# Kernel optimization log

Hardware: AMD Instinct MI355X
Metric: run time of the kernel (lower is better)

## Reference

```python
import jax, jax.numpy as jnp
import numpy as np

N = 50000
E_RAND = 800000
F_IN = 512
HID = 64
HEADS = 4
C = 40
NEG_SLOPE = 0.2  # PyG GATConv default leaky_relu slope


def setup_inputs() -> dict:
    key = jax.random.key(0)
    ks = jax.random.split(key, 12)
    x = jax.random.normal(ks[0], (N, F_IN), dtype=jnp.float32)
    # random edges + self loops (PyG GATConv add_self_loops=True)
    ei_rand = jax.random.randint(ks[1], (2, E_RAND), 0, N, dtype=jnp.int64)
    loops = jnp.broadcast_to(jnp.arange(N, dtype=jnp.int64), (2, N))
    edge_index = jnp.concatenate([ei_rand, loops], axis=1)  # [2, 850000]
    # layer 1: F_IN -> HEADS*HID, concat
    s1 = 1.0 / np.sqrt(F_IN)
    W1 = jax.random.normal(ks[2], (F_IN, HEADS * HID), dtype=jnp.float32) * s1
    a_src1 = jax.random.normal(ks[3], (HEADS, HID), dtype=jnp.float32) * (1.0 / np.sqrt(HID))
    a_dst1 = jax.random.normal(ks[4], (HEADS, HID), dtype=jnp.float32) * (1.0 / np.sqrt(HID))
    b1 = jnp.zeros((HEADS * HID,), dtype=jnp.float32)
    # layer 2: HEADS*HID -> C, 1 head, concat=False
    s2 = 1.0 / np.sqrt(HEADS * HID)
    W2 = jax.random.normal(ks[5], (HEADS * HID, C), dtype=jnp.float32) * s2
    a_src2 = jax.random.normal(ks[6], (1, C), dtype=jnp.float32) * (1.0 / np.sqrt(C))
    a_dst2 = jax.random.normal(ks[7], (1, C), dtype=jnp.float32) * (1.0 / np.sqrt(C))
    b2 = jnp.zeros((C,), dtype=jnp.float32)
    return {"x": x, "edge_index": edge_index, "W1": W1, "a_src1": a_src1,
            "a_dst1": a_dst1, "b1": b1, "W2": W2, "a_src2": a_src2,
            "a_dst2": a_dst2, "b2": b2}


def gat_conv(x, src, dst, W, a_s, a_d, b, concat):
    n = x.shape[0]
    H, D = a_s.shape
    h = (x @ W).reshape(n, H, D)                    # [N,H,D]
    al_s = jnp.einsum('nhd,hd->nh', h, a_s)          # per-node src score
    al_d = jnp.einsum('nhd,hd->nh', h, a_d)          # per-node dst score
    e = jax.nn.leaky_relu(al_s[src] + al_d[dst], NEG_SLOPE)  # [E,H]
    # segment softmax over edges grouped by destination node
    m = jax.ops.segment_max(e, dst, num_segments=n)  # [N,H]
    e = jnp.exp(e - m[dst])
    denom = jax.ops.segment_sum(e, dst, num_segments=n)
    alpha = e / (denom[dst] + 1e-16)                 # [E,H]
    msg = h[src] * alpha[:, :, None]                 # [E,H,D]
    out = jax.ops.segment_sum(msg, dst, num_segments=n)  # [N,H,D]
    out = out.reshape(n, H * D) if concat else out.mean(axis=1)
    return out + b


def reference(x, edge_index, W1, a_src1, a_dst1, b1, W2, a_src2, a_dst2, b2):
    src, dst = edge_index[0], edge_index[1]
    # dropout p=0.6 is identity in eval mode
    h = jax.nn.elu(gat_conv(x, src, dst, W1, a_src1, a_dst1, b1, concat=True))
    out = gat_conv(h, src, dst, W2, a_src2, a_dst2, b2, concat=False)
    return jax.nn.log_softmax(out, axis=1)
```

## Files before the change

kernel.cpp:

```cpp
#include <hip/hip_runtime.h>
#include <math.h>

#define NNODES 50000
#define FIN 512
#define HID 64
#define HEADS 4
#define HD (HEADS * HID)
#define NCLS 40
#define NCLSP 64
#define NEG_SLOPE 0.2f
#define SBLK 256
#define NSCAN ((NNODES + SBLK - 1) / SBLK)

#define W1TBLK (FIN * HD / 256)
#define W2TBLK NCLSP

typedef __attribute__((ext_vector_type(8))) short short8;
typedef __attribute__((ext_vector_type(4))) float f32x4;

static __device__ inline unsigned short f2bf(float f) {
    unsigned int u = __builtin_bit_cast(unsigned int, f);
    unsigned int r = (u + 0x7FFFu + ((u >> 16) & 1u)) >> 16;
    return (unsigned short)r;
}
static __device__ inline float bf2f(unsigned short b) {
    return __builtin_bit_cast(float, (unsigned int)b << 16);
}
static __device__ inline void gload_lds16(const unsigned short* g, unsigned short* l) {
    __builtin_amdgcn_global_load_lds(
        (const __attribute__((address_space(1))) unsigned int*)g,
        (__attribute__((address_space(3))) unsigned int*)l, 16, 0, 0);
}

__global__ __launch_bounds__(256) void pre_kernel(const float* __restrict__ W1,
                                                  unsigned short* __restrict__ W1t,
                                                  const float* __restrict__ W2,
                                                  unsigned short* __restrict__ W2t,
                                                  const int* __restrict__ ei, int E, int eb,
                                                  int* __restrict__ deg,
                                                  int* __restrict__ csr_pad) {
    const int b = blockIdx.x;
    const int tid = threadIdx.x;
    if (b < eb) {
        const int e = b * 256 + tid;
        if (e < E) atomicAdd(&deg[ei[E + e]], 1);
        if (b == 0 && tid < 64) csr_pad[tid] = 0;
    } else if (b < eb + W1TBLK) {
        const int idx = (b - eb) * 256 + tid;
        const int k = idx >> 8;
        const int n = idx & 255;
        W1t[n * FIN + k] = f2bf(W1[idx]);
    } else {
        const int idx = (b - eb - W1TBLK) * 256 + tid;
        const int n = idx >> 8;
        const int k = idx & 255;
        W2t[n * HD + k] = (n < NCLS) ? f2bf(W2[k * NCLS + n]) : (unsigned short)0;
    }
}

#define BM 64
#define BN 256
#define BK 32
#define G1BLK ((NNODES + BM - 1) / BM)

__global__ __launch_bounds__(256) void gemm1_kernel(const float* __restrict__ x,
                                                    const unsigned short* __restrict__ W1t,
                                                    const float* __restrict__ a_src,
                                                    const float* __restrict__ a_dst,
                                                    unsigned short* __restrict__ h1,
                                                    float* __restrict__ al_s,
                                                    float* __restrict__ al_d) {
    __shared__ unsigned short As[2][BM * BK];
    __shared__ unsigned short Bs[2][BN * BK];
    const int tid = threadIdx.x;
    const int wave = tid >> 6;
    const int lane = tid & 63;
    const int quad = lane >> 4;
    const int col = lane & 15;
    const int m0 = blockIdx.x * BM;
    const int srow = lane >> 2;
    const int skk = (lane & 3) * 8;

    const int ar = wave * 16 + srow;
    const size_t agr = (size_t)min(m0 + ar, NNODES - 1) * FIN;

    f32x4 acc[4][4] = {};

    auto stageB = [&](int buf, int k0) {
        #pragma unroll
        for (int c = 0; c < 4; ++c) {
            const int rr = c * 64 + wave * 16 + srow;
            gload_lds16(&W1t[(size_t)rr * FIN + k0 + skk], &Bs[buf][rr * BK + skk]);
        }
    };
    auto stageA = [&](int buf, int k0) {
        const float4 v0 = *(const float4*)&x[agr + k0 + skk];
        const float4 v1 = *(const float4*)&x[agr + k0 + skk + 4];
        short8 p;
        p[0] = (short)f2bf(v0.x); p[1] = (short)f2bf(v0.y);
        p[2] = (short)f2bf(v0.z); p[3] = (short)f2bf(v0.w);
        p[4] = (short)f2bf(v1.x); p[5] = (short)f2bf(v1.y);
        p[6] = (short)f2bf(v1.z); p[7] = (short)f2bf(v1.w);
        *(short8*)&As[buf][ar * BK + skk] = p;
    };
    auto compute = [&](int buf) {
        short8 af[4], bfv[4];
        #pragma unroll
        for (int i = 0; i < 4; ++i)
            af[i] = *(const short8*)&As[buf][(i * 16 + col) * BK + quad * 8];
        #pragma unroll
        for (int j = 0; j < 4; ++j)
            bfv[j] = *(const short8*)&Bs[buf][(wave * 64 + j * 16 + col) * BK + quad * 8];
        #pragma unroll
        for (int i = 0; i < 4; ++i)
            #pragma unroll
            for (int j = 0; j < 4; ++j)
                acc[i][j] = __builtin_amdgcn_mfma_f32_16x16x32_bf16(af[i], bfv[j], acc[i][j], 0, 0, 0);
    };

    stageB(0, 0);
    stageA(0, 0);
    __syncthreads();
    int cur = 0;
    for (int k0 = BK; k0 < FIN; k0 += BK) {
        stageB(cur ^ 1, k0);
        stageA(cur ^ 1, k0);
        compute(cur);
        __syncthreads();
        cur ^= 1;
    }
    compute(cur);

    float asv[4], adv[4];
    #pragma unroll
    for (int j = 0; j < 4; ++j) {
        asv[j] = a_src[wave * 64 + j * 16 + col];
        adv[j] = a_dst[wave * 64 + j * 16 + col];
    }
    #pragma unroll
    for (int i = 0; i < 4; ++i) {
        #pragma unroll
        for (int reg = 0; reg < 4; ++reg) {
            const int row = i * 16 + quad * 4 + reg;
            const int gm = m0 + row;
            float ds = 0.f, dd = 0.f;
            #pragma unroll
            for (int j = 0; j < 4; ++j) {
                const float v = acc[i][j][reg];
                ds = fmaf(v, asv[j], ds);
                dd = fmaf(v, adv[j], dd);
                if (gm < NNODES) {
                    const int gc = wave * 64 + j * 16 + col;
                    h1[(size_t)gm * HD + gc] = f2bf(v);
                }
            }
            #pragma unroll
            for (int off = 1; off < 16; off <<= 1) {
                ds += __shfl_xor(ds, off);
                dd += __shfl_xor(dd, off);
            }
            if (col == 0 && gm < NNODES) {
                al_s[gm * HEADS + wave] = ds;
                al_d[gm * HEADS + wave] = dd;
            }
        }
    }
}

__global__ __launch_bounds__(SBLK) void scan1_kernel(const int* __restrict__ deg,
                                                     int* __restrict__ psum,
                                                     int* __restrict__ bsum) {
    __shared__ int ws[4];
    const int t = threadIdx.x;
    const int idx = blockIdx.x * SBLK + t;
    const int lane = t & 63;
    const int w = t >> 6;
    int sv = (idx < NNODES) ? deg[idx] : 0;
    #pragma unroll
    for (int off = 1; off < 64; off <<= 1) {
        const int n = __shfl_up(sv, off);
        if (lane >= off) sv += n;
    }
    if (lane == 63) ws[w] = sv;
    __syncthreads();
    int add = 0;
    for (int i = 0; i < w; ++i) add += ws[i];
    sv += add;
    if (idx < NNODES) psum[idx] = sv;
    if (t == SBLK - 1) bsum[blockIdx.x] = sv;
}

__global__ __launch_bounds__(SBLK) void scan23_kernel(const int* __restrict__ deg,
                                                      const int* __restrict__ psum,
                                                      const int* __restrict__ bsum,
                                                      int* __restrict__ offsets) {
    __shared__ int ws[4];
    __shared__ int sc[NSCAN];
    const int t = threadIdx.x;
    const int lane = t & 63;
    const int w = t >> 6;
    int sv = (t < NSCAN) ? bsum[t] : 0;
    #pragma unroll
    for (int off = 1; off < 64; off <<= 1) {
        const int n = __shfl_up(sv, off);
        if (lane >= off) sv += n;
    }
    if (lane == 63) ws[w] = sv;
    __syncthreads();
    int add = 0;
    for (int i = 0; i < w; ++i) add += ws[i];
    sv += add;
    if (t < NSCAN) sc[t] = sv;
    __syncthreads();
    const int idx = blockIdx.x * SBLK + t;
    const int boff = (blockIdx.x > 0) ? sc[blockIdx.x - 1] : 0;
    if (idx < NNODES) offsets[idx] = psum[idx] - deg[idx] + boff;
    if (blockIdx.x == 0 && t == 0) offsets[NNODES] = sc[NSCAN - 1];
}

__global__ void scatter_kernel(const int* __restrict__ ei, int E,
                               const int* __restrict__ offsets,
                               int* __restrict__ cursor,
                               int* __restrict__ csr_src) {
    const int e = blockIdx.x * 256 + threadIdx.x;
    if (e < E) {
        const int dst = ei[E + e];
        const int src = ei[e];
        const int pos = offsets[dst] + atomicAdd(&cursor[dst], 1);
        csr_src[pos] = src;
    }
}

__global__ __launch_bounds__(256) void agg1_kernel(const unsigned short* __restrict__ h1,
                                                   const float* __restrict__ al_s,
                                                   const float* __restrict__ al_d,
                                                   const int* __restrict__ offsets,
                                                   const int* __restrict__ csr_src,
                                                   const float* __restrict__ b1,
                                                   unsigned short* __restrict__ h_act) {
    const int node = (blockIdx.x * 256 + threadIdx.x) >> 6;
    const int lane = threadIdx.x & 63;
    const int q = lane >> 4;
    const int fl = lane & 15;
    const int h = fl >> 2;
    const float ad = al_d[node * HEADS + h];
    const int start = offsets[node];
    const int end = offsets[node + 1];

    float s = 0.f;
    float acc[16] = {};

    {
        const int idx = start + q;
        const int src0 = csr_src[idx];
        float sc = (idx < end) ? al_s[src0 * HEADS + h] : -__builtin_inff();
        short8 v0 = *(const short8*)&h1[(size_t)src0 * HD + fl * 16];
        short8 v1 = *(const short8*)&h1[(size_t)src0 * HD + fl * 16 + 8];

        for (int i = start; i < end; i += 4) {
            const int j = i + 4 + q;
            const int nsrc = csr_src[j];
            const float nsc = (j < end) ? al_s[nsrc * HEADS + h] : -__builtin_inff();
            const short8 nv0 = *(const short8*)&h1[(size_t)nsrc * HD + fl * 16];
            const short8 nv1 = *(const short8*)&h1[(size_t)nsrc * HD + fl * 16 + 8];
            float e_ = sc + ad;
            e_ = e_ > 0.f ? e_ : NEG_SLOPE * e_;
            const float p = __expf(e_);
            s += p;
            #pragma unroll
            for (int k = 0; k < 8; ++k)
                acc[k] = fmaf(p, bf2f((unsigned short)v0[k]), acc[k]);
            #pragma unroll
            for (int k = 0; k < 8; ++k)
                acc[8 + k] = fmaf(p, bf2f((unsigned short)v1[k]), acc[8 + k]);
            sc = nsc; v0 = nv0; v1 = nv1;
        }
    }
    s += __shfl_xor(s, 16);
    s += __shfl_xor(s, 32);
    #pragma unroll
    for (int k = 0; k < 16; ++k) {
        acc[k] += __shfl_xor(acc[k], 16);
        acc[k] += __shfl_xor(acc[k], 32);
    }

    if (q == 0) {
        const float inv = 1.f / (s + 1e-16f);
        float bb[16];
        *(float4*)&bb[0]  = *(const float4*)&b1[fl * 16];
        *(float4*)&bb[4]  = *(const float4*)&b1[fl * 16 + 4];
        *(float4*)&bb[8]  = *(const float4*)&b1[fl * 16 + 8];
        *(float4*)&bb[12] = *(const float4*)&b1[fl * 16 + 12];
        short8 ob0, ob1;
        #pragma unroll
        for (int k = 0; k < 8; ++k) {
            const float o0 = acc[k] * inv + bb[k];
            const float o1 = acc[8 + k] * inv + bb[8 + k];
            const float e0 = o0 > 0.f ? o0 : expm1f(o0);
            const float e1 = o1 > 0.f ? o1 : expm1f(o1);
            ob0[k] = (short)f2bf(e0);
            ob1[k] = (short)f2bf(e1);
        }
        *(short8*)&h_act[(size_t)node * HD + fl * 16] = ob0;
        *(short8*)&h_act[(size_t)node * HD + fl * 16 + 8] = ob1;
    }
}

#define G2M 64
#define BSTRIDE 264

__global__ __launch_bounds__(256) void gemm2_kernel(const unsigned short* __restrict__ h_act,
                                                    const unsigned short* __restrict__ W2t,
                                                    const float* __restrict__ a_s2,
                                                    const float* __restrict__ a_d2,
                                                    unsigned short* __restrict__ h2,
                                                    float* __restrict__ al_s,
                                                    float* __restrict__ al_d) {
    __shared__ unsigned short Bt[NCLSP][BSTRIDE];
    const int tid = threadIdx.x;
    const int wave = tid >> 6;
    const int lane = tid & 63;
    const int quad = lane >> 4;
    const int col = lane & 15;
    const int m0 = blockIdx.x * G2M;

    #pragma unroll
    for (int it = 0; it < 8; ++it) {
        const int ch = it * 256 + tid;
        const int n = ch >> 5;
        const int c8 = (ch & 31) * 8;
        *(uint4*)&Bt[n][c8] = *(const uint4*)&W2t[(size_t)n * HD + c8];
    }

    const int rowm = m0 + wave * 16 + col;
    const int arow = min(rowm, NNODES - 1);
    short8 af[8];
    #pragma unroll
    for (int ks = 0; ks < 8; ++ks)
        af[ks] = *(const short8*)&h_act[(size_t)arow * HD + ks * 32 + quad * 8];

    __syncthreads();

    f32x4 acc[4] = {};
    #pragma unroll
    for (int j = 0; j < 4; ++j) {
        #pragma unroll
        for (int ks = 0; ks < 8; ++ks) {
            const short8 bfr = *(const short8*)&Bt[j * 16 + col][ks * 32 + quad * 8];
            acc[j] = __builtin_amdgcn_mfma_f32_16x16x32_bf16(af[ks], bfr, acc[j], 0, 0, 0);
        }
    }

    float ps[4] = {0.f, 0.f, 0.f, 0.f};
    float pd[4] = {0.f, 0.f, 0.f, 0.f};
    #pragma unroll
    for (int j = 0; j < 4; ++j) {
        const int c = j * 16 + col;
        const bool cv = c < NCLS;
        const float asc = cv ? a_s2[c] : 0.f;
        const float adc = cv ? a_d2[c] : 0.f;
        #pragma unroll
        for (int reg = 0; reg < 4; ++reg) {
            const float v = acc[j][reg];
            ps[reg] += v * asc;
            pd[reg] += v * adc;
            const int node = m0 + wave * 16 + quad * 4 + reg;
            if (node < NNODES)
                h2[(size_t)node * NCLSP + c] = f2bf(v);
        }
    }
    #pragma unroll
    for (int reg = 0; reg < 4; ++reg) {
        #pragma unroll
        for (int off = 1; off < 16; off <<= 1) {
            ps[reg] += __shfl_xor(ps[reg], off);
            pd[reg] += __shfl_xor(pd[reg], off);
        }
    }
    if (col == 0) {
        #pragma unroll
        for (int reg = 0; reg < 4; ++reg) {
            const int node = m0 + wave * 16 + quad * 4 + reg;
            if (node < NNODES) {
                al_s[node] = ps[reg];
                al_d[node] = pd[reg];
            }
        }
    }
}

__global__ __launch_bounds__(256) void agg2_kernel(const unsigned short* __restrict__ h2,
                                                   const float* __restrict__ al_s,
                                                   const float* __restrict__ al_d,
                                                   const int* __restrict__ offsets,
                                                   const int* __restrict__ csr_src,
                                                   const float* __restrict__ b2,
                                                   float* __restrict__ out) {
    const int node = (blockIdx.x * 256 + threadIdx.x) >> 6;
    const int lane = threadIdx.x & 63;
    const int oct = lane >> 3;
    const int fl = lane & 7;
    const float ad = al_d[node];
    const int start = offsets[node];
    const int end = offsets[node + 1];

    float s = 0.f;
    float acc[8] = {};

    {
        const int idx = start + oct;
        const int src0 = csr_src[idx];
        float sc = (idx < end) ? al_s[src0] : -__builtin_inff();
        short8 v = *(const short8*)&h2[(size_t)src0 * NCLSP + fl * 8];

        for (int i = start; i < end; i += 8) {
            const int j = i + 8 + oct;
            const int nsrc = csr_src[j];
            const float nsc = (j < end) ? al_s[nsrc] : -__builtin_inff();
            const short8 nv = *(const short8*)&h2[(size_t)nsrc * NCLSP + fl * 8];
            float e_ = sc + ad;
            e_ = e_ > 0.f ? e_ : NEG_SLOPE * e_;
            const float p = __expf(e_);
            s += p;
            #pragma unroll
            for (int k = 0; k < 8; ++k)
                acc[k] = fmaf(p, bf2f((unsigned short)v[k]), acc[k]);
            sc = nsc; v = nv;
        }
    }
    s += __shfl_xor(s, 8);
    s += __shfl_xor(s, 16);
    s += __shfl_xor(s, 32);
    #pragma unroll
    for (int k = 0; k < 8; ++k) {
        acc[k] += __shfl_xor(acc[k], 8);
        acc[k] += __shfl_xor(acc[k], 16);
        acc[k] += __shfl_xor(acc[k], 32);
    }

    if (oct == 0) {
        const float inv = 1.f / (s + 1e-16f);
        float o[8];
        float mx = -1e30f;
        #pragma unroll
        for (int k = 0; k < 8; ++k) {
            const int c = fl * 8 + k;
            const float bc = (c < NCLS) ? b2[c] : 0.f;
            o[k] = acc[k] * inv + bc;
            if (c < NCLS) mx = fmaxf(mx, o[k]);
        }
        #pragma unroll
        for (int off = 1; off < 8; off <<= 1) mx = fmaxf(mx, __shfl_xor(mx, off));
        float ex = 0.f;
        #pragma unroll
        for (int k = 0; k < 8; ++k) {
            const int c = fl * 8 + k;
            if (c < NCLS) ex += __expf(o[k] - mx);
        }
        #pragma unroll
        for (int off = 1; off < 8; off <<= 1) ex += __shfl_xor(ex, off);
        const float lse = mx + logf(ex);
        if (fl < 5) {
            float4 r0, r1;
            r0.x = o[0] - lse; r0.y = o[1] - lse; r0.z = o[2] - lse; r0.w = o[3] - lse;
            r1.x = o[4] - lse; r1.y = o[5] - lse; r1.z = o[6] - lse; r1.w = o[7] - lse;
            *(float4*)&out[(size_t)node * NCLS + fl * 8] = r0;
            *(float4*)&out[(size_t)node * NCLS + fl * 8 + 4] = r1;
        }
    }
}

extern "C" void kernel_launch(void* const* d_in, const int* in_sizes, int n_in,
                              void* d_out, int out_size, void* d_ws, size_t ws_size,
                              hipStream_t stream) {
    const float* x      = (const float*)d_in[0];
    const int*   ei     = (const int*)d_in[1];
    const float* W1     = (const float*)d_in[2];
    const float* a_src1 = (const float*)d_in[3];
    const float* a_dst1 = (const float*)d_in[4];
    const float* b1     = (const float*)d_in[5];
    const float* W2     = (const float*)d_in[6];
    const float* a_src2 = (const float*)d_in[7];
    const float* a_dst2 = (const float*)d_in[8];
    const float* b2     = (const float*)d_in[9];
    float* out = (float*)d_out;
    const int E = in_sizes[1] / 2;

    char* ws = (char*)d_ws;
    size_t off = 0;
    auto alloc = [&](size_t bytes) -> char* {
        char* p = ws + off;
        off += (bytes + 255) & ~(size_t)255;
        return p;
    };
    unsigned short* W1t   = (unsigned short*)alloc((size_t)FIN * HD * 2);
    unsigned short* W2t   = (unsigned short*)alloc((size_t)NCLSP * HD * 2);
    unsigned short* h1    = (unsigned short*)alloc((size_t)NNODES * HD * 2);
    unsigned short* h_act = (unsigned short*)alloc((size_t)NNODES * HD * 2);
    unsigned short* h2    = (unsigned short*)alloc((size_t)NNODES * NCLSP * 2);
    float* al_s1  = (float*)alloc((size_t)NNODES * HEADS * 4);
    float* al_d1  = (float*)alloc((size_t)NNODES * HEADS * 4);
    float* al_s2  = (float*)alloc((size_t)NNODES * 4);
    float* al_d2  = (float*)alloc((size_t)NNODES * 4);
    int*   deg    = (int*)alloc((size_t)NNODES * 4);
    int*   cursor = (int*)alloc((size_t)NNODES * 4);
    int*   psum   = (int*)alloc((size_t)NNODES * 4);
    int*   bsum   = (int*)alloc((size_t)SBLK * 4);
    int*   offs   = (int*)alloc((size_t)(NNODES + 1) * 4);
    int*   csrsrc = (int*)alloc((size_t)E * 4 + 256);

    const size_t degpad = ((size_t)NNODES * 4 + 255) & ~(size_t)255;
    hipMemsetAsync(deg, 0, degpad + (size_t)NNODES * 4, stream);

    const int eb = (E + 255) / 256;
    pre_kernel<<<eb + W1TBLK + W2TBLK, 256, 0, stream>>>(W1, W1t, W2, W2t, ei, E, eb, deg, csrsrc + E);
    scan1_kernel<<<NSCAN, SBLK, 0, stream>>>(deg, psum, bsum);
    scan23_kernel<<<NSCAN, SBLK, 0, stream>>>(deg, psum, bsum, offs);
    scatter_kernel<<<eb, 256, 0, stream>>>(ei, E, offs, cursor, csrsrc);

    gemm1_kernel<<<G1BLK, 256, 0, stream>>>(x, W1t, a_src1, a_dst1, h1, al_s1, al_d1);
    agg1_kernel<<<NNODES / 4, 256, 0, stream>>>(h1, al_s1, al_d1, offs, csrsrc, b1, h_act);
    gemm2_kernel<<<(NNODES + G2M - 1) / G2M, 256, 0, stream>>>(h_act, W2t, a_src2, a_dst2, h2, al_s2, al_d2);
    agg2_kernel<<<NNODES / 4, 256, 0, stream>>>(h2, al_s2, al_d2, offs, csrsrc, b2, out);
}
```

Baseline: 405.8 us.

## Stage fp32 x tile via direct global-to-LDS loads with XOR swizzle; cheaper bf16 unpack

The first GEMM now loads the fp32 input tile straight into LDS with asynchronous global_load_lds and an XOR-swizzled layout, and converts to bf16 when fragments are read rather than in registers before the LDS store. This takes the A-operand global loads off the VGPR path and lets them overlap with compute like the B tile does, at the price of twice the LDS footprint for A and conversion work repeated inside the compute loop. Separately, the layer-1 aggregation kernel unpacks bf16 pairs from 32-bit words with shift and mask instead of extracting individual shorts, which cuts unpack instructions.

New measurement: 401.1 us. About the same (-1.2%).

```diff
diff --git a/kernel.cpp b/kernel.cpp
--- a/kernel.cpp
+++ b/kernel.cpp
@@ -26,7 +26,7 @@
 static __device__ inline float bf2f(unsigned short b) {
     return __builtin_bit_cast(float, (unsigned int)b << 16);
 }
-static __device__ inline void gload_lds16(const unsigned short* g, unsigned short* l) {
+static __device__ inline void gload_lds16(const void* g, void* l) {
     __builtin_amdgcn_global_load_lds(
         (const __attribute__((address_space(1))) unsigned int*)g,
         (__attribute__((address_space(3))) unsigned int*)l, 16, 0, 0);
@@ -70,7 +70,7 @@
                                                     unsigned short* __restrict__ h1,
                                                     float* __restrict__ al_s,
                                                     float* __restrict__ al_d) {
-    __shared__ unsigned short As[2][BM * BK];
+    __shared__ float As32[2][BM * BK];
     __shared__ unsigned short Bs[2][BN * BK];
     const int tid = threadIdx.x;
     const int wave = tid >> 6;
@@ -80,12 +80,20 @@
     const int m0 = blockIdx.x * BM;
     const int srow = lane >> 2;
     const int skk = (lane & 3) * 8;
-
-    const int ar = wave * 16 + srow;
-    const size_t agr = (size_t)min(m0 + ar, NNODES - 1) * FIN;
+    const int l3 = lane >> 3;
+    const int ch = lane & 7;
+    const int chs = ch ^ l3;
 
     f32x4 acc[4][4] = {};
 
+    auto stageA = [&](int buf, int k0) {
+        #pragma unroll
+        for (int j = 0; j < 2; ++j) {
+            const int row = wave * 16 + j * 8 + l3;
+            const size_t rg = (size_t)min(m0 + row, NNODES - 1) * FIN;
+            gload_lds16(&x[rg + k0 + chs * 4], &As32[buf][row * BK + ch * 4]);
+        }
+    };
     auto stageB = [&](int buf, int k0) {
         #pragma unroll
         for (int c = 0; c < 4; ++c) {
@@ -93,21 +101,21 @@
             gload_lds16(&W1t[(size_t)rr * FIN + k0 + skk], &Bs[buf][rr * BK + skk]);
         }
     };
-    auto stageA = [&](int buf, int k0) {
-        const float4 v0 = *(const float4*)&x[agr + k0 + skk];
-        const float4 v1 = *(const float4*)&x[agr + k0 + skk + 4];
-        short8 p;
-        p[0] = (short)f2bf(v0.x); p[1] = (short)f2bf(v0.y);
-        p[2] = (short)f2bf(v0.z); p[3] = (short)f2bf(v0.w);
-        p[4] = (short)f2bf(v1.x); p[5] = (short)f2bf(v1.y);
-        p[6] = (short)f2bf(v1.z); p[7] = (short)f2bf(v1.w);
-        *(short8*)&As[buf][ar * BK + skk] = p;
-    };
     auto compute = [&](int buf) {
+        const int r7 = col & 7;
         short8 af[4], bfv[4];
         #pragma unroll
-        for (int i = 0; i < 4; ++i)
-            af[i] = *(const short8*)&As[buf][(i * 16 + col) * BK + quad * 8];
+        for (int i = 0; i < 4; ++i) {
+            const int row = i * 16 + col;
+            const float4 f0 = *(const float4*)&As32[buf][row * BK + (((2 * quad)     ^ r7) << 2)];
+            const float4 f1 = *(const float4*)&As32[buf][row * BK + (((2 * quad + 1) ^ r7) << 2)];
+            short8 p;
+            p[0] = (short)f2bf(f0.x); p[1] = (short)f2bf(f0.y);
+            p[2] = (short)f2bf(f0.z); p[3] = (short)f2bf(f0.w);
+            p[4] = (short)f2bf(f1.x); p[5] = (short)f2bf(f1.y);
+            p[6] = (short)f2bf(f1.z); p[7] = (short)f2bf(f1.w);
+            af[i] = p;
+        }
         #pragma unroll
         for (int j = 0; j < 4; ++j)
             bfv[j] = *(const short8*)&Bs[buf][(wave * 64 + j * 16 + col) * BK + quad * 8];
@@ -118,13 +126,13 @@
                 acc[i][j] = __builtin_amdgcn_mfma_f32_16x16x32_bf16(af[i], bfv[j], acc[i][j], 0, 0, 0);
     };
 
+    stageA(0, 0);
     stageB(0, 0);
-    stageA(0, 0);
     __syncthreads();
     int cur = 0;
     for (int k0 = BK; k0 < FIN; k0 += BK) {
+        stageA(cur ^ 1, k0);
         stageB(cur ^ 1, k0);
-        stageA(cur ^ 1, k0);
         compute(cur);
         __syncthreads();
         cur ^= 1;
@@ -254,25 +262,27 @@
         const int idx = start + q;
         const int src0 = csr_src[idx];
         float sc = (idx < end) ? al_s[src0 * HEADS + h] : -__builtin_inff();
-        short8 v0 = *(const short8*)&h1[(size_t)src0 * HD + fl * 16];
-        short8 v1 = *(const short8*)&h1[(size_t)src0 * HD + fl * 16 + 8];
+        uint4 v0 = *(const uint4*)&h1[(size_t)src0 * HD + fl * 16];
+        uint4 v1 = *(const uint4*)&h1[(size_t)src0 * HD + fl * 16 + 8];
 
         for (int i = start; i < end; i += 4) {
             const int j = i + 4 + q;
             const int nsrc = csr_src[j];
             const float nsc = (j < end) ? al_s[nsrc * HEADS + h] : -__builtin_inff();
-            const short8 nv0 = *(const short8*)&h1[(size_t)nsrc * HD + fl * 16];
-            const short8 nv1 = *(const short8*)&h1[(size_t)nsrc * HD + fl * 16 + 8];
+            const uint4 nv0 = *(const uint4*)&h1[(size_t)nsrc * HD + fl * 16];
+            const uint4 nv1 = *(const uint4*)&h1[(size_t)nsrc * HD + fl * 16 + 8];
             float e_ = sc + ad;
             e_ = e_ > 0.f ? e_ : NEG_SLOPE * e_;
             const float p = __expf(e_);
             s += p;
+            const unsigned int w[8] = {v0.x, v0.y, v0.z, v0.w, v1.x, v1.y, v1.z, v1.w};
             #pragma unroll
-            for (int k = 0; k < 8; ++k)
-                acc[k] = fmaf(p, bf2f((unsigned short)v0[k]), acc[k]);
-            #pragma unroll
-            for (int k = 0; k < 8; ++k)
-                acc[8 + k] = fmaf(p, bf2f((unsigned short)v1[k]), acc[8 + k]);
+            for (int d = 0; d < 8; ++d) {
+                const float lo = __builtin_bit_cast(float, w[d] << 16);
+                const float hi = __builtin_bit_cast(float, w[d] & 0xFFFF0000u);
+                acc[2 * d]     = fmaf(p, lo, acc[2 * d]);
+                acc[2 * d + 1] = fmaf(p, hi, acc[2 * d + 1]);
+            }
             sc = nsc; v0 = nv0; v1 = nv1;
         }
     }
```
